# Kernel tuning notes

Measured on AMD Instinct MI355X. Metric: run time of the kernel, lower is better.

## Reference

```python
import jax, jax.numpy as jnp
import numpy as np

N, E, G = 131072, 2097152, 512
IN, H = 64, 2
C1, C2 = 32, 64
EDIM = 3
EPS = 1e-5


def setup_inputs() -> dict:
    key = jax.random.key(0)
    ks = jax.random.split(key, 32)
    p = lambda k, shp, s=0.1: (jax.random.normal(k, shp, dtype=jnp.float32) * s)
    inp = {
        'x': jax.random.normal(ks[0], (N, IN), dtype=jnp.float32),
        'edge_attr': jax.random.normal(ks[1], (E, EDIM), dtype=jnp.float32),
        # layer 1 (in=64 -> H*C1=64)
        'w1l': p(ks[2], (IN, H * C1)), 'b1l': p(ks[3], (H * C1,)),
        'w1r': p(ks[4], (IN, H * C1)), 'b1r': p(ks[5], (H * C1,)),
        'w1e': p(ks[6], (EDIM, H * C1)),
        'att1': p(ks[7], (H, C1)), 'bias1': p(ks[8], (C1,)),
        'g1': jnp.ones((C1,), jnp.float32), 'be1': jnp.zeros((C1,), jnp.float32),
        # layer 2 (in=32 -> H*C2=128)
        'w2l': p(ks[9], (C1, H * C2)), 'b2l': p(ks[10], (H * C2,)),
        'w2r': p(ks[11], (C1, H * C2)), 'b2r': p(ks[12], (H * C2,)),
        'w2e': p(ks[13], (EDIM, H * C2)),
        'att2': p(ks[14], (H, C2)), 'bias2': p(ks[15], (C2,)),
        'g2': jnp.ones((C2,), jnp.float32), 'be2': jnp.zeros((C2,), jnp.float32),
        # head
        'fc1w': p(ks[16], (C2, 32)), 'fc1b': p(ks[17], (32,)),
        'g3': jnp.ones((32,), jnp.float32), 'be3': jnp.zeros((32,), jnp.float32),
        'fc2w': p(ks[18], (32, 1)), 'fc2b': p(ks[19], (1,)),
        # graph structure (int)
        'edge_index': jax.random.randint(ks[20], (2, E), 0, N, dtype=jnp.int32),
        'batch': jnp.sort(jax.random.randint(ks[21], (N,), 0, G, dtype=jnp.int32)),
    }
    return inp


def _seg_softmax(logits, seg, n):
    # numerically stable segment softmax over edges grouped by dst node
    m = jax.ops.segment_max(logits, seg, num_segments=n)
    m = jnp.where(jnp.isfinite(m), m, 0.0)
    e = jnp.exp(logits - m[seg])
    s = jax.ops.segment_sum(e, seg, num_segments=n)
    return e / (s[seg] + 1e-16)


def _gatv2(x, src, dst, eattr, wl, bl, wr, br, we, att, bias, heads, ch):
    n = x.shape[0]
    xl = (x @ wl + bl).reshape(n, heads, ch)            # lin_l (source side)
    xr = (x @ wr + br).reshape(n, heads, ch)            # lin_r (target side)
    ee = (eattr @ we).reshape(-1, heads, ch)            # edge embedding
    m = jax.nn.leaky_relu(xl[src] + xr[dst] + ee, 0.2)  # [Etot,H,C]
    logits = jnp.einsum('ehc,hc->eh', m, att)           # [Etot,H]
    alpha = _seg_softmax(logits, dst, n)                # [Etot,H]
    out = jax.ops.segment_sum(alpha[:, :, None] * xl[src], dst, num_segments=n)
    return out.mean(axis=1) + bias                      # concat=False -> head mean


def _bn(x, g, b):
    mu = x.mean(0)
    v = x.var(0)
    return (x - mu) * jax.lax.rsqrt(v + EPS) * g + b


def reference(x, edge_attr, w1l, b1l, w1r, b1r, w1e, att1, bias1, g1, be1,
              w2l, b2l, w2r, b2r, w2e, att2, bias2, g2, be2,
              fc1w, fc1b, g3, be3, fc2w, fc2b, edge_index, batch):
    n = x.shape[0]
    src, dst = edge_index[0], edge_index[1]
    # add self loops with fill_value='mean' edge attrs (PyG default)
    cnt = jax.ops.segment_sum(jnp.ones_like(dst, jnp.float32), dst, num_segments=n)
    loop_attr = jax.ops.segment_sum(edge_attr, dst, num_segments=n) / jnp.maximum(cnt, 1.0)[:, None]
    ar = jnp.arange(n, dtype=src.dtype)
    src_f = jnp.concatenate([src, ar])
    dst_f = jnp.concatenate([dst, ar])
    ea_f = jnp.concatenate([edge_attr, loop_attr], axis=0)

    h = _gatv2(x, src_f, dst_f, ea_f, w1l, b1l, w1r, b1r, w1e, att1, bias1, H, C1)
    h = jax.nn.elu(_bn(h, g1, be1))
    h = _gatv2(h, src_f, dst_f, ea_f, w2l, b2l, w2r, b2r, w2e, att2, bias2, H, C2)
    h = jax.nn.elu(_bn(h, g2, be2))

    # global mean pool over graphs
    gs = jax.ops.segment_sum(h, batch, num_segments=G)
    gc = jax.ops.segment_sum(jnp.ones((n,), jnp.float32), batch, num_segments=G)
    pooled = gs / jnp.maximum(gc, 1.0)[:, None]

    z = jax.nn.elu(_bn(pooled @ fc1w + fc1b, g3, be3))
    return jax.nn.sigmoid(z @ fc2w + fc2b)
```

## Files before the change

### kernel.cpp

```cpp
#include <hip/hip_runtime.h>
#include <math.h>

#define NN 131072
#define EE 2097152
#define ET (EE + NN)
#define GG 512
#define BN_EPS 1e-5f

__device__ __forceinline__ unsigned short f2bf(float f) {
  unsigned u = __float_as_uint(f);
  u += 0x7fffu + ((u >> 16) & 1u);
  return (unsigned short)(u >> 16);
}
__device__ __forceinline__ float bf_lo(unsigned u) {
  return __uint_as_float(u << 16);
}
__device__ __forceinline__ float bf_hi(unsigned u) {
  return __uint_as_float(u & 0xffff0000u);
}

__global__ void k_hist(const int* __restrict__ ei, int* __restrict__ cnt,
                       int* __restrict__ rank) {
  int e = blockIdx.x * blockDim.x + threadIdx.x;
  if (e >= EE) return;
  rank[e] = atomicAdd(&cnt[ei[EE + e]], 1);
}

__global__ void k_scan_a(const int* __restrict__ cnt, int* __restrict__ off_out,
                         int* __restrict__ bsum) {
  __shared__ int s[256];
  int i = blockIdx.x * 256 + threadIdx.x;
  int x = cnt[i] + 1;
  s[threadIdx.x] = x;
  __syncthreads();
#pragma unroll
  for (int o = 1; o < 256; o <<= 1) {
    int t = (threadIdx.x >= o) ? s[threadIdx.x - o] : 0;
    __syncthreads();
    s[threadIdx.x] += t;
    __syncthreads();
  }
  off_out[i] = s[threadIdx.x] - x;
  if (threadIdx.x == 255) bsum[blockIdx.x] = s[255];
}

__global__ void k_scan_b(int* __restrict__ bsum) {
  __shared__ int s[512];
  int t = threadIdx.x;
  int x = bsum[t];
  s[t] = x;
  __syncthreads();
#pragma unroll
  for (int o = 1; o < 512; o <<= 1) {
    int v = (t >= o) ? s[t - o] : 0;
    __syncthreads();
    s[t] += v;
    __syncthreads();
  }
  bsum[t] = s[t] - x;
}

__global__ void k_scan_c(int* __restrict__ off_out, const int* __restrict__ bsum) {
  int i = blockIdx.x * 256 + threadIdx.x;
  off_out[i] += bsum[blockIdx.x];
  if (i == 0) off_out[NN] = ET;
}

__global__ void k_scatter(const int* __restrict__ ei, const float* __restrict__ ea,
                          const int* __restrict__ off, const int* __restrict__ rank,
                          float4* __restrict__ ces) {
  int e = blockIdx.x * blockDim.x + threadIdx.x;
  if (e >= EE) return;
  int s = ei[e], d = ei[EE + e];
  int p = off[d] + rank[e];
  float4 t = {ea[3 * e], ea[3 * e + 1], ea[3 * e + 2], __int_as_float(s)};
  ces[p] = t;
}

__global__ void k_selfslot(const int* __restrict__ off, float4* __restrict__ ces) {
  int tid = blockIdx.x * blockDim.x + threadIdx.x;
  int wave = tid >> 6;
  int lane = threadIdx.x & 63;
  int grp = lane >> 4;
  int gl = lane & 15;
  int v = wave * 4 + grp;
  if (v >= NN) return;
  int b = off[v];
  int d = off[v + 1] - b - 1;
  float s0 = 0.f, s1 = 0.f, s2 = 0.f;
  for (int j = gl; j < d; j += 16) {
    float4 t = ces[b + j];
    s0 += t.x;
    s1 += t.y;
    s2 += t.z;
  }
#pragma unroll
  for (int m = 1; m <= 8; m <<= 1) {
    s0 += __shfl_xor(s0, m, 64);
    s1 += __shfl_xor(s1, m, 64);
    s2 += __shfl_xor(s2, m, 64);
  }
  if (gl == 0) {
    float inv = 1.0f / (float)(d > 0 ? d : 1);
    float4 t = {s0 * inv, s1 * inv, s2 * inv, __int_as_float(v)};
    ces[b + d] = t;
  }
}

template <int K, int O, bool DO_BN>
__global__ void k_lin(const float* __restrict__ x, const float* __restrict__ wl,
                      const float* __restrict__ bl, const float* __restrict__ wr,
                      const float* __restrict__ br, unsigned short* __restrict__ xlb,
                      float* __restrict__ xr, const float* __restrict__ bnsum,
                      const float* __restrict__ bnss, const float* __restrict__ g,
                      const float* __restrict__ be) {
  constexpr int NPB = 256 / O;
  __shared__ float swl[K * O], swr[K * O], sx[NPB * K];
  __shared__ float sscale[K], sshift[K];
  for (int i = threadIdx.x; i < K * O; i += 256) {
    swl[i] = wl[i];
    swr[i] = wr[i];
  }
  if (DO_BN && threadIdx.x < K) {
    int c = threadIdx.x;
    float mu = bnsum[c] * (1.0f / NN);
    float var = bnss[c] * (1.0f / NN) - mu * mu;
    float is = rsqrtf(var + BN_EPS) * g[c];
    sscale[c] = is;
    sshift[c] = be[c] - mu * is;
  }
  int o = threadIdx.x % O;
  int ln = threadIdx.x / O;
  float blv = bl[o], brv = br[o];
  __syncthreads();
  for (int v0 = blockIdx.x * NPB; v0 < NN; v0 += gridDim.x * NPB) {
    __syncthreads();
    for (int i = threadIdx.x; i < NPB * K; i += 256) {
      float xv = x[(size_t)v0 * K + i];
      if (DO_BN) {
        int c = i & (K - 1);
        xv = xv * sscale[c] + sshift[c];
        xv = (xv > 0.0f) ? xv : (__expf(xv) - 1.0f);
      }
      sx[i] = xv;
    }
    __syncthreads();
    float al = blv, ar = brv;
#pragma unroll 8
    for (int k = 0; k < K; k++) {
      float xv = sx[ln * K + k];
      al += xv * swl[k * O + o];
      ar += xv * swr[k * O + o];
    }
    int v = v0 + ln;
    xlb[(size_t)v * O + o] = f2bf(al);
    xr[(size_t)v * O + o] = ar;
  }
}


__global__ void k_gat128(const int* __restrict__ off, const float4* __restrict__ ces,
                         const uint2* __restrict__ xlb, const float4* __restrict__ xr,
                         const float4* __restrict__ we, const float4* __restrict__ att,
                         const float4* __restrict__ bias, float4* __restrict__ hout,
                         float* __restrict__ bnsum, float* __restrict__ bnss) {
  __shared__ float lsum[4][64], lsq[4][64];
  int lane = threadIdx.x & 63;
  int wid = threadIdx.x >> 6;
  int cl = lane & 31;
  int half = lane >> 5;
  const float4 w0 = we[cl], w1 = we[32 + cl], w2 = we[64 + cl];
  const float4 av = att[cl];
  float4 rs = {0, 0, 0, 0}, rq = {0, 0, 0, 0};
  for (int v = blockIdx.x * 4 + wid; v < NN; v += gridDim.x * 4) {
    int b = off[v], e = off[v + 1];
    int last = e - 1;
    float4 xrv = xr[(size_t)v * 32 + cl];
    float ssum = 0.0f;
    float4 acc = {0, 0, 0, 0};
    int ng = (e - b + 3) >> 2;
    int j = b;
    float4 pa = ces[min(j + half, last)];
    float4 pb = ces[min(j + 2 + half, last)];
    uint2 ua = xlb[(size_t)__float_as_int(pa.w) * 32 + cl];
    uint2 ub = xlb[(size_t)__float_as_int(pb.w) * 32 + cl];
    float4 qa = ces[min(j + 4 + half, last)];
    float4 qb = ces[min(j + 6 + half, last)];
    for (int g = 0; g < ng; g++, j += 4) {
      uint2 nua = xlb[(size_t)__float_as_int(qa.w) * 32 + cl];
      uint2 nub = xlb[(size_t)__float_as_int(qb.w) * 32 + cl];
      float4 ta = ces[min(j + 8 + half, last)];
      float4 tb = ces[min(j + 10 + half, last)];
      float4 ra, rb;
      ra.x = bf_lo(ua.x); ra.y = bf_hi(ua.x); ra.z = bf_lo(ua.y); ra.w = bf_hi(ua.y);
      rb.x = bf_lo(ub.x); rb.y = bf_hi(ub.x); rb.z = bf_lo(ub.y); rb.w = bf_hi(ub.y);
      float4 ma, mb;
      ma.x = ra.x + xrv.x + pa.x * w0.x + pa.y * w1.x + pa.z * w2.x;
      ma.y = ra.y + xrv.y + pa.x * w0.y + pa.y * w1.y + pa.z * w2.y;
      ma.z = ra.z + xrv.z + pa.x * w0.z + pa.y * w1.z + pa.z * w2.z;
      ma.w = ra.w + xrv.w + pa.x * w0.w + pa.y * w1.w + pa.z * w2.w;
      mb.x = rb.x + xrv.x + pb.x * w0.x + pb.y * w1.x + pb.z * w2.x;
      mb.y = rb.y + xrv.y + pb.x * w0.y + pb.y * w1.y + pb.z * w2.y;
      mb.z = rb.z + xrv.z + pb.x * w0.z + pb.y * w1.z + pb.z * w2.z;
      mb.w = rb.w + xrv.w + pb.x * w0.w + pb.y * w1.w + pb.z * w2.w;
      ma.x = fmaxf(ma.x, 0.2f * ma.x); ma.y = fmaxf(ma.y, 0.2f * ma.y);
      ma.z = fmaxf(ma.z, 0.2f * ma.z); ma.w = fmaxf(ma.w, 0.2f * ma.w);
      mb.x = fmaxf(mb.x, 0.2f * mb.x); mb.y = fmaxf(mb.y, 0.2f * mb.y);
      mb.z = fmaxf(mb.z, 0.2f * mb.z); mb.w = fmaxf(mb.w, 0.2f * mb.w);
      float la = ma.x * av.x + ma.y * av.y + ma.z * av.z + ma.w * av.w;
      float lb = mb.x * av.x + mb.y * av.y + mb.z * av.z + mb.w * av.w;
#pragma unroll
      for (int m = 1; m <= 8; m <<= 1) {
        la += __shfl_xor(la, m, 64);
        lb += __shfl_xor(lb, m, 64);
      }
      float pA = ((j + half) < e) ? __expf(la) : 0.0f;
      float pB = ((j + 2 + half) < e) ? __expf(lb) : 0.0f;
      ssum += pA + pB;
      acc.x += pA * ra.x + pB * rb.x;
      acc.y += pA * ra.y + pB * rb.y;
      acc.z += pA * ra.z + pB * rb.z;
      acc.w += pA * ra.w + pB * rb.w;
      pa = qa; pb = qb; ua = nua; ub = nub; qa = ta; qb = tb;
    }
    ssum += __shfl_xor(ssum, 32, 64);
    acc.x += __shfl_xor(acc.x, 32, 64);
    acc.y += __shfl_xor(acc.y, 32, 64);
    acc.z += __shfl_xor(acc.z, 32, 64);
    acc.w += __shfl_xor(acc.w, 32, 64);
    float inv = 1.0f / (ssum + 1e-16f);
    float4 o = {acc.x * inv, acc.y * inv, acc.z * inv, acc.w * inv};
    float px = __shfl_xor(o.x, 16, 64);
    float py = __shfl_xor(o.y, 16, 64);
    float pz = __shfl_xor(o.z, 16, 64);
    float pw = __shfl_xor(o.w, 16, 64);
    if (lane < 16) {
      float4 bv = bias[lane];
      float4 val = {0.5f * (o.x + px) + bv.x, 0.5f * (o.y + py) + bv.y,
                    0.5f * (o.z + pz) + bv.z, 0.5f * (o.w + pw) + bv.w};
      hout[(size_t)v * 16 + lane] = val;
      rs.x += val.x; rs.y += val.y; rs.z += val.z; rs.w += val.w;
      rq.x += val.x * val.x; rq.y += val.y * val.y;
      rq.z += val.z * val.z; rq.w += val.w * val.w;
    }
  }
  if (lane < 16) {
    lsum[wid][4 * lane] = rs.x; lsum[wid][4 * lane + 1] = rs.y;
    lsum[wid][4 * lane + 2] = rs.z; lsum[wid][4 * lane + 3] = rs.w;
    lsq[wid][4 * lane] = rq.x; lsq[wid][4 * lane + 1] = rq.y;
    lsq[wid][4 * lane + 2] = rq.z; lsq[wid][4 * lane + 3] = rq.w;
  }
  __syncthreads();
  if (threadIdx.x < 64) {
    float a = lsum[0][threadIdx.x] + lsum[1][threadIdx.x] + lsum[2][threadIdx.x] +
              lsum[3][threadIdx.x];
    float q = lsq[0][threadIdx.x] + lsq[1][threadIdx.x] + lsq[2][threadIdx.x] +
              lsq[3][threadIdx.x];
    atomicAdd(&bnsum[threadIdx.x], a);
    atomicAdd(&bnss[threadIdx.x], q);
  }
}

__global__ void k_gat64(const int* __restrict__ off, const float4* __restrict__ ces,
                        const unsigned* __restrict__ xlb, const float2* __restrict__ xr,
                        const float2* __restrict__ we, const float2* __restrict__ att,
                        const float2* __restrict__ bias, float2* __restrict__ hout,
                        float* __restrict__ bnsum, float* __restrict__ bnss) {
  __shared__ float lsum[4][32], lsq[4][32];
  int lane = threadIdx.x & 63;
  int wid = threadIdx.x >> 6;
  int cl = lane & 31;
  int half = lane >> 5;
  const float2 w0 = we[cl], w1 = we[32 + cl], w2 = we[64 + cl];
  const float2 av = att[cl];
  float2 rs = {0, 0}, rq = {0, 0};
  for (int v = blockIdx.x * 4 + wid; v < NN; v += gridDim.x * 4) {
    int b = off[v], e = off[v + 1];
    int last = e - 1;
    float2 xrv = xr[(size_t)v * 32 + cl];
    float ssum = 0.0f;
    float2 acc = {0, 0};
    int ng = (e - b + 3) >> 2;
    int j = b;
    float4 pa = ces[min(j + half, last)];
    float4 pb = ces[min(j + 2 + half, last)];
    unsigned ua = xlb[(size_t)__float_as_int(pa.w) * 32 + cl];
    unsigned ub = xlb[(size_t)__float_as_int(pb.w) * 32 + cl];
    float4 qa = ces[min(j + 4 + half, last)];
    float4 qb = ces[min(j + 6 + half, last)];
    for (int g = 0; g < ng; g++, j += 4) {
      unsigned nua = xlb[(size_t)__float_as_int(qa.w) * 32 + cl];
      unsigned nub = xlb[(size_t)__float_as_int(qb.w) * 32 + cl];
      float4 ta = ces[min(j + 8 + half, last)];
      float4 tb = ces[min(j + 10 + half, last)];
      float2 ra = {bf_lo(ua), bf_hi(ua)};
      float2 rb = {bf_lo(ub), bf_hi(ub)};
      float2 ma, mb;
      ma.x = ra.x + xrv.x + pa.x * w0.x + pa.y * w1.x + pa.z * w2.x;
      ma.y = ra.y + xrv.y + pa.x * w0.y + pa.y * w1.y + pa.z * w2.y;
      mb.x = rb.x + xrv.x + pb.x * w0.x + pb.y * w1.x + pb.z * w2.x;
      mb.y = rb.y + xrv.y + pb.x * w0.y + pb.y * w1.y + pb.z * w2.y;
      ma.x = fmaxf(ma.x, 0.2f * ma.x); ma.y = fmaxf(ma.y, 0.2f * ma.y);
      mb.x = fmaxf(mb.x, 0.2f * mb.x); mb.y = fmaxf(mb.y, 0.2f * mb.y);
      float la = ma.x * av.x + ma.y * av.y;
      float lb = mb.x * av.x + mb.y * av.y;
#pragma unroll
      for (int m = 1; m <= 8; m <<= 1) {
        la += __shfl_xor(la, m, 64);
        lb += __shfl_xor(lb, m, 64);
      }
      float pA = ((j + half) < e) ? __expf(la) : 0.0f;
      float pB = ((j + 2 + half) < e) ? __expf(lb) : 0.0f;
      ssum += pA + pB;
      acc.x += pA * ra.x + pB * rb.x;
      acc.y += pA * ra.y + pB * rb.y;
      pa = qa; pb = qb; ua = nua; ub = nub; qa = ta; qb = tb;
    }
    ssum += __shfl_xor(ssum, 32, 64);
    acc.x += __shfl_xor(acc.x, 32, 64);
    acc.y += __shfl_xor(acc.y, 32, 64);
    float inv = 1.0f / (ssum + 1e-16f);
    float2 o = {acc.x * inv, acc.y * inv};
    float px = __shfl_xor(o.x, 16, 64);
    float py = __shfl_xor(o.y, 16, 64);
    if (lane < 16) {
      float2 bv = bias[lane];
      float2 val = {0.5f * (o.x + px) + bv.x, 0.5f * (o.y + py) + bv.y};
      hout[(size_t)v * 16 + lane] = val;
      rs.x += val.x; rs.y += val.y;
      rq.x += val.x * val.x; rq.y += val.y * val.y;
    }
  }
  if (lane < 16) {
    lsum[wid][2 * lane] = rs.x; lsum[wid][2 * lane + 1] = rs.y;
    lsq[wid][2 * lane] = rq.x; lsq[wid][2 * lane + 1] = rq.y;
  }
  __syncthreads();
  if (threadIdx.x < 32) {
    float a = lsum[0][threadIdx.x] + lsum[1][threadIdx.x] + lsum[2][threadIdx.x] +
              lsum[3][threadIdx.x];
    float q = lsq[0][threadIdx.x] + lsq[1][threadIdx.x] + lsq[2][threadIdx.x] +
              lsq[3][threadIdx.x];
    atomicAdd(&bnsum[threadIdx.x], a);
    atomicAdd(&bnss[threadIdx.x], q);
  }
}

__global__ void k_goffbs(const int* __restrict__ batch, int* __restrict__ goff) {
  int g = threadIdx.x;
  int lo = 0, hi = NN;
  while (lo < hi) {
    int mid = (lo + hi) >> 1;
    if (batch[mid] < g) lo = mid + 1; else hi = mid;
  }
  goff[g] = lo;
  if (g == 0) goff[GG] = NN;
}

__global__ void k_pool(const float* __restrict__ h2, const int* __restrict__ goff,
                       const float* __restrict__ bnsum, const float* __restrict__ bnss,
                       const float* __restrict__ g, const float* __restrict__ be,
                       float* __restrict__ pooled) {
  int gi = blockIdx.x, c = threadIdx.x;
  float mu = bnsum[c] * (1.0f / NN);
  float var = bnss[c] * (1.0f / NN) - mu * mu;
  float is = rsqrtf(var + BN_EPS) * g[c];
  float sh = be[c] - mu * is;
  int s = goff[gi], n = goff[gi + 1] - s;
  float acc = 0.0f;
  int i = 0;
  for (; i + 4 <= n; i += 4) {
    float y0 = h2[(size_t)(s + i) * 64 + c];
    float y1 = h2[(size_t)(s + i + 1) * 64 + c];
    float y2 = h2[(size_t)(s + i + 2) * 64 + c];
    float y3 = h2[(size_t)(s + i + 3) * 64 + c];
    y0 = y0 * is + sh; y1 = y1 * is + sh; y2 = y2 * is + sh; y3 = y3 * is + sh;
    y0 = (y0 > 0.0f) ? y0 : (__expf(y0) - 1.0f);
    y1 = (y1 > 0.0f) ? y1 : (__expf(y1) - 1.0f);
    y2 = (y2 > 0.0f) ? y2 : (__expf(y2) - 1.0f);
    y3 = (y3 > 0.0f) ? y3 : (__expf(y3) - 1.0f);
    acc += (y0 + y1) + (y2 + y3);
  }
  for (; i < n; i++) {
    float y = h2[(size_t)(s + i) * 64 + c] * is + sh;
    y = (y > 0.0f) ? y : (__expf(y) - 1.0f);
    acc += y;
  }
  pooled[gi * 64 + c] = acc / fmaxf((float)n, 1.0f);
}

__global__ void k_fc1(const float* __restrict__ pooled, const float* __restrict__ w,
                      const float* __restrict__ b, float* __restrict__ t1) {
  int i = blockIdx.x * blockDim.x + threadIdx.x;
  int g = i >> 5, o = i & 31;
  float acc = b[o];
#pragma unroll 8
  for (int k = 0; k < 64; k++) acc += pooled[g * 64 + k] * w[k * 32 + o];
  t1[i] = acc;
}

__global__ void k_head(const float* __restrict__ t1, const float* __restrict__ g3,
                       const float* __restrict__ be3, const float* __restrict__ fc2w,
                       const float* __restrict__ fc2b, float* __restrict__ out) {
  __shared__ float ssum[32], ssq[32], smu[32], sinv[32];
  int t = threadIdx.x;
  if (t < 32) {
    ssum[t] = 0.0f;
    ssq[t] = 0.0f;
  }
  __syncthreads();
  float y[32];
#pragma unroll
  for (int o = 0; o < 32; o++) y[o] = t1[t * 32 + o];
#pragma unroll
  for (int o = 0; o < 32; o++) {
    atomicAdd(&ssum[o], y[o]);
    atomicAdd(&ssq[o], y[o] * y[o]);
  }
  __syncthreads();
  if (t < 32) {
    float mu = ssum[t] * (1.0f / GG);
    float var = ssq[t] * (1.0f / GG) - mu * mu;
    smu[t] = mu;
    sinv[t] = rsqrtf(var + BN_EPS);
  }
  __syncthreads();
  float acc = fc2b[0];
#pragma unroll
  for (int o = 0; o < 32; o++) {
    float yy = (y[o] - smu[o]) * sinv[o] * g3[o] + be3[o];
    yy = (yy > 0.0f) ? yy : (__expf(yy) - 1.0f);
    acc += yy * fc2w[o];
  }
  out[t] = 1.0f / (1.0f + __expf(-acc));
}

extern "C" void kernel_launch(void* const* d_in, const int* in_sizes, int n_in,
                              void* d_out, int out_size, void* d_ws, size_t ws_size,
                              hipStream_t stream) {
  const float* x = (const float*)d_in[0];
  const float* ea = (const float*)d_in[1];
  const float* w1l = (const float*)d_in[2];
  const float* b1l = (const float*)d_in[3];
  const float* w1r = (const float*)d_in[4];
  const float* b1r = (const float*)d_in[5];
  const float* w1e = (const float*)d_in[6];
  const float* att1 = (const float*)d_in[7];
  const float* bias1 = (const float*)d_in[8];
  const float* g1 = (const float*)d_in[9];
  const float* be1 = (const float*)d_in[10];
  const float* w2l = (const float*)d_in[11];
  const float* b2l = (const float*)d_in[12];
  const float* w2r = (const float*)d_in[13];
  const float* b2r = (const float*)d_in[14];
  const float* w2e = (const float*)d_in[15];
  const float* att2 = (const float*)d_in[16];
  const float* bias2 = (const float*)d_in[17];
  const float* g2 = (const float*)d_in[18];
  const float* be2 = (const float*)d_in[19];
  const float* fc1w = (const float*)d_in[20];
  const float* fc1b = (const float*)d_in[21];
  const float* g3 = (const float*)d_in[22];
  const float* be3 = (const float*)d_in[23];
  const float* fc2w = (const float*)d_in[24];
  const float* fc2b = (const float*)d_in[25];
  const int* ei = (const int*)d_in[26];
  const int* batch = (const int*)d_in[27];
  float* out = (float*)d_out;

  char* w = (char*)d_ws;
  size_t off = 0;
  auto alloc = [&](size_t bytes) {
    size_t r = off;
    off += (bytes + 255) & ~(size_t)255;
    return r;
  };
  int* cnt = (int*)(w + alloc(NN * 4));
  float* bn1sum = (float*)(w + alloc(32 * 4));
  float* bn1ss = (float*)(w + alloc(32 * 4));
  float* bn2sum = (float*)(w + alloc(64 * 4));
  float* bn2ss = (float*)(w + alloc(64 * 4));
  size_t zero_bytes = off;
  int* rank = (int*)(w + alloc((size_t)EE * 4));
  int* csr_off = (int*)(w + alloc((size_t)(NN + 1) * 4));
  int* bsum = (int*)(w + alloc(512 * 4));
  int* goff = (int*)(w + alloc((size_t)(GG + 1) * 4));
  float4* ces = (float4*)(w + alloc((size_t)ET * 16));
  unsigned short* xlb = (unsigned short*)(w + alloc((size_t)NN * 128 * 2));
  float* xr = (float*)(w + alloc((size_t)NN * 128 * 4));
  float* h1 = (float*)(w + alloc((size_t)NN * 32 * 4));
  float* h2 = (float*)(w + alloc((size_t)NN * 64 * 4));
  float* pooled = (float*)(w + alloc((size_t)GG * 64 * 4));
  float* t1 = (float*)(w + alloc((size_t)GG * 32 * 4));
  (void)ws_size;
  (void)in_sizes;
  (void)n_in;
  (void)out_size;

  hipMemsetAsync(d_ws, 0, zero_bytes, stream);

  k_hist<<<EE / 256, 256, 0, stream>>>(ei, cnt, rank);
  k_scan_a<<<512, 256, 0, stream>>>(cnt, csr_off, bsum);
  k_scan_b<<<1, 512, 0, stream>>>(bsum);
  k_scan_c<<<512, 256, 0, stream>>>(csr_off, bsum);
  k_scatter<<<EE / 256, 256, 0, stream>>>(ei, ea, csr_off, rank, ces);
  k_selfslot<<<NN / 16, 256, 0, stream>>>(csr_off, ces);

  k_lin<64, 64, false><<<2048, 256, 0, stream>>>(x, w1l, b1l, w1r, b1r, xlb, xr,
                                                 nullptr, nullptr, nullptr, nullptr);
  k_gat64<<<2048, 256, 0, stream>>>(csr_off, ces, (const unsigned*)xlb,
                                    (const float2*)xr, (const float2*)w1e,
                                    (const float2*)att1, (const float2*)bias1,
                                    (float2*)h1, bn1sum, bn1ss);

  k_lin<32, 128, true><<<2048, 256, 0, stream>>>(h1, w2l, b2l, w2r, b2r, xlb, xr,
                                                 bn1sum, bn1ss, g1, be1);
  k_gat128<<<2048, 256, 0, stream>>>(csr_off, ces, (const uint2*)xlb,
                                     (const float4*)xr, (const float4*)w2e,
                                     (const float4*)att2, (const float4*)bias2,
                                     (float4*)h2, bn2sum, bn2ss);

  k_goffbs<<<1, GG, 0, stream>>>(batch, goff);
  k_pool<<<GG, 64, 0, stream>>>(h2, goff, bn2sum, bn2ss, g2, be2, pooled);
  k_fc1<<<64, 256, 0, stream>>>(pooled, fc1w, fc1b, t1);
  k_head<<<1, GG, 0, stream>>>(t1, g3, be3, fc2w, fc2b, out);
}
```

Measured before the change: 990.2 us.

## Remap GAT aggregation lanes to 16 per edge with wider vector gathers

Both GAT aggregation kernels now give 16 lanes to each edge and process four edges per wave at once, instead of 32 lanes per edge with two edges per half-wave. Each lane loads wider bf16 and fp32 vectors, which cuts the per-edge attention-logit reduction to three shuffles. The min() clamping on prefetch indices is removed; instead the CSR edge array gets 16 zeroed padding slots, so prefetches past the end stay in bounds and stray edges are masked by the jj<e check. This trades more registers per lane (two float4 accumulators in the 128-wide kernel) for fewer shuffle and index instructions and better-coalesced gathers.

```diff
diff --git a/kernel.cpp b/kernel.cpp
--- a/kernel.cpp
+++ b/kernel.cpp
@@ -12,12 +12,8 @@
   u += 0x7fffu + ((u >> 16) & 1u);
   return (unsigned short)(u >> 16);
 }
-__device__ __forceinline__ float bf_lo(unsigned u) {
-  return __uint_as_float(u << 16);
-}
-__device__ __forceinline__ float bf_hi(unsigned u) {
-  return __uint_as_float(u & 0xffff0000u);
-}
+__device__ __forceinline__ float bf_lo(unsigned u) { return __uint_as_float(u << 16); }
+__device__ __forceinline__ float bf_hi(unsigned u) { return __uint_as_float(u & 0xffff0000u); }
 
 __global__ void k_hist(const int* __restrict__ ei, int* __restrict__ cnt,
                        int* __restrict__ rank) {
@@ -79,6 +75,10 @@
 
 __global__ void k_selfslot(const int* __restrict__ off, float4* __restrict__ ces) {
   int tid = blockIdx.x * blockDim.x + threadIdx.x;
+  if (tid < 16) {
+    float4 z = {0.0f, 0.0f, 0.0f, __int_as_float(0)};
+    ces[ET + tid] = z;
+  }
   int wave = tid >> 6;
   int lane = threadIdx.x & 63;
   int grp = lane >> 4;
@@ -160,95 +160,101 @@
 
 
 __global__ void k_gat128(const int* __restrict__ off, const float4* __restrict__ ces,
-                         const uint2* __restrict__ xlb, const float4* __restrict__ xr,
+                         const uint4* __restrict__ xlb, const float4* __restrict__ xr,
                          const float4* __restrict__ we, const float4* __restrict__ att,
                          const float4* __restrict__ bias, float4* __restrict__ hout,
                          float* __restrict__ bnsum, float* __restrict__ bnss) {
   __shared__ float lsum[4][64], lsq[4][64];
   int lane = threadIdx.x & 63;
   int wid = threadIdx.x >> 6;
-  int cl = lane & 31;
-  int half = lane >> 5;
-  const float4 w0 = we[cl], w1 = we[32 + cl], w2 = we[64 + cl];
-  const float4 av = att[cl];
-  float4 rs = {0, 0, 0, 0}, rq = {0, 0, 0, 0};
+  int el = lane & 15;
+  int st = lane >> 4;
+  const float4 w0a = we[el * 2], w0b = we[el * 2 + 1];
+  const float4 w1a = we[32 + el * 2], w1b = we[32 + el * 2 + 1];
+  const float4 w2a = we[64 + el * 2], w2b = we[64 + el * 2 + 1];
+  const float4 ava = att[el * 2], avb = att[el * 2 + 1];
+  float4 rsa = {0, 0, 0, 0}, rsb = {0, 0, 0, 0};
+  float4 rqa = {0, 0, 0, 0}, rqb = {0, 0, 0, 0};
   for (int v = blockIdx.x * 4 + wid; v < NN; v += gridDim.x * 4) {
     int b = off[v], e = off[v + 1];
-    int last = e - 1;
-    float4 xrv = xr[(size_t)v * 32 + cl];
+    float4 xra = xr[(size_t)v * 32 + el * 2];
+    float4 xrb = xr[(size_t)v * 32 + el * 2 + 1];
     float ssum = 0.0f;
-    float4 acc = {0, 0, 0, 0};
+    float4 acca = {0, 0, 0, 0}, accb = {0, 0, 0, 0};
     int ng = (e - b + 3) >> 2;
-    int j = b;
-    float4 pa = ces[min(j + half, last)];
-    float4 pb = ces[min(j + 2 + half, last)];
-    uint2 ua = xlb[(size_t)__float_as_int(pa.w) * 32 + cl];
-    uint2 ub = xlb[(size_t)__float_as_int(pb.w) * 32 + cl];
-    float4 qa = ces[min(j + 4 + half, last)];
-    float4 qb = ces[min(j + 6 + half, last)];
-    for (int g = 0; g < ng; g++, j += 4) {
-      uint2 nua = xlb[(size_t)__float_as_int(qa.w) * 32 + cl];
-      uint2 nub = xlb[(size_t)__float_as_int(qb.w) * 32 + cl];
-      float4 ta = ces[min(j + 8 + half, last)];
-      float4 tb = ces[min(j + 10 + half, last)];
+    int jj = b + st;
+    float4 pa = ces[jj];
+    uint4 ua = xlb[(size_t)__float_as_int(pa.w) * 16 + el];
+    float4 qa = ces[jj + 4];
+    for (int g = 0; g < ng; g++) {
+      uint4 nua = xlb[(size_t)__float_as_int(qa.w) * 16 + el];
+      float4 ta = ces[jj + 8];
       float4 ra, rb;
       ra.x = bf_lo(ua.x); ra.y = bf_hi(ua.x); ra.z = bf_lo(ua.y); ra.w = bf_hi(ua.y);
-      rb.x = bf_lo(ub.x); rb.y = bf_hi(ub.x); rb.z = bf_lo(ub.y); rb.w = bf_hi(ub.y);
+      rb.x = bf_lo(ua.z); rb.y = bf_hi(ua.z); rb.z = bf_lo(ua.w); rb.w = bf_hi(ua.w);
       float4 ma, mb;
-      ma.x = ra.x + xrv.x + pa.x * w0.x + pa.y * w1.x + pa.z * w2.x;
-      ma.y = ra.y + xrv.y + pa.x * w0.y + pa.y * w1.y + pa.z * w2.y;
-      ma.z = ra.z + xrv.z + pa.x * w0.z + pa.y * w1.z + pa.z * w2.z;
-      ma.w = ra.w + xrv.w + pa.x * w0.w + pa.y * w1.w + pa.z * w2.w;
-      mb.x = rb.x + xrv.x + pb.x * w0.x + pb.y * w1.x + pb.z * w2.x;
-      mb.y = rb.y + xrv.y + pb.x * w0.y + pb.y * w1.y + pb.z * w2.y;
-      mb.z = rb.z + xrv.z + pb.x * w0.z + pb.y * w1.z + pb.z * w2.z;
-      mb.w = rb.w + xrv.w + pb.x * w0.w + pb.y * w1.w + pb.z * w2.w;
+      ma.x = ra.x + xra.x + pa.x * w0a.x + pa.y * w1a.x + pa.z * w2a.x;
+      ma.y = ra.y + xra.y + pa.x * w0a.y + pa.y * w1a.y + pa.z * w2a.y;
+      ma.z = ra.z + xra.z + pa.x * w0a.z + pa.y * w1a.z + pa.z * w2a.z;
+      ma.w = ra.w + xra.w + pa.x * w0a.w + pa.y * w1a.w + pa.z * w2a.w;
+      mb.x = rb.x + xrb.x + pa.x * w0b.x + pa.y * w1b.x + pa.z * w2b.x;
+      mb.y = rb.y + xrb.y + pa.x * w0b.y + pa.y * w1b.y + pa.z * w2b.y;
+      mb.z = rb.z + xrb.z + pa.x * w0b.z + pa.y * w1b.z + pa.z * w2b.z;
+      mb.w = rb.w + xrb.w + pa.x * w0b.w + pa.y * w1b.w + pa.z * w2b.w;
       ma.x = fmaxf(ma.x, 0.2f * ma.x); ma.y = fmaxf(ma.y, 0.2f * ma.y);
       ma.z = fmaxf(ma.z, 0.2f * ma.z); ma.w = fmaxf(ma.w, 0.2f * ma.w);
       mb.x = fmaxf(mb.x, 0.2f * mb.x); mb.y = fmaxf(mb.y, 0.2f * mb.y);
       mb.z = fmaxf(mb.z, 0.2f * mb.z); mb.w = fmaxf(mb.w, 0.2f * mb.w);
-      float la = ma.x * av.x + ma.y * av.y + ma.z * av.z + ma.w * av.w;
-      float lb = mb.x * av.x + mb.y * av.y + mb.z * av.z + mb.w * av.w;
-#pragma unroll
-      for (int m = 1; m <= 8; m <<= 1) {
-        la += __shfl_xor(la, m, 64);
-        lb += __shfl_xor(lb, m, 64);
-      }
-      float pA = ((j + half) < e) ? __expf(la) : 0.0f;
-      float pB = ((j + 2 + half) < e) ? __expf(lb) : 0.0f;
-      ssum += pA + pB;
-      acc.x += pA * ra.x + pB * rb.x;
-      acc.y += pA * ra.y + pB * rb.y;
-      acc.z += pA * ra.z + pB * rb.z;
-      acc.w += pA * ra.w + pB * rb.w;
-      pa = qa; pb = qb; ua = nua; ub = nub; qa = ta; qb = tb;
-    }
-    ssum += __shfl_xor(ssum, 32, 64);
-    acc.x += __shfl_xor(acc.x, 32, 64);
-    acc.y += __shfl_xor(acc.y, 32, 64);
-    acc.z += __shfl_xor(acc.z, 32, 64);
-    acc.w += __shfl_xor(acc.w, 32, 64);
+      float l = ma.x * ava.x + ma.y * ava.y + ma.z * ava.z + ma.w * ava.w +
+                mb.x * avb.x + mb.y * avb.y + mb.z * avb.z + mb.w * avb.w;
+      l += __shfl_xor(l, 1, 64);
+      l += __shfl_xor(l, 2, 64);
+      l += __shfl_xor(l, 4, 64);
+      float p = (jj < e) ? __expf(l) : 0.0f;
+      ssum += p;
+      acca.x += p * ra.x; acca.y += p * ra.y; acca.z += p * ra.z; acca.w += p * ra.w;
+      accb.x += p * rb.x; accb.y += p * rb.y; accb.z += p * rb.z; accb.w += p * rb.w;
+      jj += 4;
+      pa = qa; ua = nua; qa = ta;
+    }
+#pragma unroll
+    for (int m = 16; m <= 32; m <<= 1) {
+      ssum += __shfl_xor(ssum, m, 64);
+      acca.x += __shfl_xor(acca.x, m, 64); acca.y += __shfl_xor(acca.y, m, 64);
+      acca.z += __shfl_xor(acca.z, m, 64); acca.w += __shfl_xor(acca.w, m, 64);
+      accb.x += __shfl_xor(accb.x, m, 64); accb.y += __shfl_xor(accb.y, m, 64);
+      accb.z += __shfl_xor(accb.z, m, 64); accb.w += __shfl_xor(accb.w, m, 64);
+    }
     float inv = 1.0f / (ssum + 1e-16f);
-    float4 o = {acc.x * inv, acc.y * inv, acc.z * inv, acc.w * inv};
-    float px = __shfl_xor(o.x, 16, 64);
-    float py = __shfl_xor(o.y, 16, 64);
-    float pz = __shfl_xor(o.z, 16, 64);
-    float pw = __shfl_xor(o.w, 16, 64);
-    if (lane < 16) {
-      float4 bv = bias[lane];
-      float4 val = {0.5f * (o.x + px) + bv.x, 0.5f * (o.y + py) + bv.y,
-                    0.5f * (o.z + pz) + bv.z, 0.5f * (o.w + pw) + bv.w};
-      hout[(size_t)v * 16 + lane] = val;
-      rs.x += val.x; rs.y += val.y; rs.z += val.z; rs.w += val.w;
-      rq.x += val.x * val.x; rq.y += val.y * val.y;
-      rq.z += val.z * val.z; rq.w += val.w * val.w;
-    }
-  }
-  if (lane < 16) {
-    lsum[wid][4 * lane] = rs.x; lsum[wid][4 * lane + 1] = rs.y;
-    lsum[wid][4 * lane + 2] = rs.z; lsum[wid][4 * lane + 3] = rs.w;
-    lsq[wid][4 * lane] = rq.x; lsq[wid][4 * lane + 1] = rq.y;
-    lsq[wid][4 * lane + 2] = rq.z; lsq[wid][4 * lane + 3] = rq.w;
+    float4 oa = {acca.x * inv, acca.y * inv, acca.z * inv, acca.w * inv};
+    float4 ob = {accb.x * inv, accb.y * inv, accb.z * inv, accb.w * inv};
+    float pax = __shfl_xor(oa.x, 8, 64), pay = __shfl_xor(oa.y, 8, 64);
+    float paz = __shfl_xor(oa.z, 8, 64), paw = __shfl_xor(oa.w, 8, 64);
+    float pbx = __shfl_xor(ob.x, 8, 64), pby = __shfl_xor(ob.y, 8, 64);
+    float pbz = __shfl_xor(ob.z, 8, 64), pbw = __shfl_xor(ob.w, 8, 64);
+    if (lane < 8) {
+      float4 bva = bias[el * 2], bvb = bias[el * 2 + 1];
+      float4 va = {0.5f * (oa.x + pax) + bva.x, 0.5f * (oa.y + pay) + bva.y,
+                   0.5f * (oa.z + paz) + bva.z, 0.5f * (oa.w + paw) + bva.w};
+      float4 vb = {0.5f * (ob.x + pbx) + bvb.x, 0.5f * (ob.y + pby) + bvb.y,
+                   0.5f * (ob.z + pbz) + bvb.z, 0.5f * (ob.w + pbw) + bvb.w};
+      hout[(size_t)v * 16 + el * 2] = va;
+      hout[(size_t)v * 16 + el * 2 + 1] = vb;
+      rsa.x += va.x; rsa.y += va.y; rsa.z += va.z; rsa.w += va.w;
+      rsb.x += vb.x; rsb.y += vb.y; rsb.z += vb.z; rsb.w += vb.w;
+      rqa.x += va.x * va.x; rqa.y += va.y * va.y; rqa.z += va.z * va.z; rqa.w += va.w * va.w;
+      rqb.x += vb.x * vb.x; rqb.y += vb.y * vb.y; rqb.z += vb.z * vb.z; rqb.w += vb.w * vb.w;
+    }
+  }
+  if (lane < 8) {
+    lsum[wid][el * 8 + 0] = rsa.x; lsum[wid][el * 8 + 1] = rsa.y;
+    lsum[wid][el * 8 + 2] = rsa.z; lsum[wid][el * 8 + 3] = rsa.w;
+    lsum[wid][el * 8 + 4] = rsb.x; lsum[wid][el * 8 + 5] = rsb.y;
+    lsum[wid][el * 8 + 6] = rsb.z; lsum[wid][el * 8 + 7] = rsb.w;
+    lsq[wid][el * 8 + 0] = rqa.x; lsq[wid][el * 8 + 1] = rqa.y;
+    lsq[wid][el * 8 + 2] = rqa.z; lsq[wid][el * 8 + 3] = rqa.w;
+    lsq[wid][el * 8 + 4] = rqb.x; lsq[wid][el * 8 + 5] = rqb.y;
+    lsq[wid][el * 8 + 6] = rqb.z; lsq[wid][el * 8 + 7] = rqb.w;
   }
   __syncthreads();
   if (threadIdx.x < 64) {
@@ -262,78 +268,75 @@
 }
 
 __global__ void k_gat64(const int* __restrict__ off, const float4* __restrict__ ces,
-                        const unsigned* __restrict__ xlb, const float2* __restrict__ xr,
-                        const float2* __restrict__ we, const float2* __restrict__ att,
-                        const float2* __restrict__ bias, float2* __restrict__ hout,
+                        const uint2* __restrict__ xlb, const float4* __restrict__ xr,
+                        const float4* __restrict__ we, const float4* __restrict__ att,
+                        const float4* __restrict__ bias, float4* __restrict__ hout,
                         float* __restrict__ bnsum, float* __restrict__ bnss) {
   __shared__ float lsum[4][32], lsq[4][32];
   int lane = threadIdx.x & 63;
   int wid = threadIdx.x >> 6;
-  int cl = lane & 31;
-  int half = lane >> 5;
-  const float2 w0 = we[cl], w1 = we[32 + cl], w2 = we[64 + cl];
-  const float2 av = att[cl];
-  float2 rs = {0, 0}, rq = {0, 0};
+  int el = lane & 15;
+  int st = lane >> 4;
+  const float4 w0 = we[el], w1 = we[16 + el], w2 = we[32 + el];
+  const float4 av = att[el];
+  float4 rs = {0, 0, 0, 0}, rq = {0, 0, 0, 0};
   for (int v = blockIdx.x * 4 + wid; v < NN; v += gridDim.x * 4) {
     int b = off[v], e = off[v + 1];
-    int last = e - 1;
-    float2 xrv = xr[(size_t)v * 32 + cl];
+    float4 xrv = xr[(size_t)v * 16 + el];
     float ssum = 0.0f;
-    float2 acc = {0, 0};
+    float4 acc = {0, 0, 0, 0};
     int ng = (e - b + 3) >> 2;
-    int j = b;
-    float4 pa = ces[min(j + half, last)];
-    float4 pb = ces[min(j + 2 + half, last)];
-    unsigned ua = xlb[(size_t)__float_as_int(pa.w) * 32 + cl];
-    unsigned ub = xlb[(size_t)__float_as_int(pb.w) * 32 + cl];
-    float4 qa = ces[min(j + 4 + half, last)];
-    float4 qb = ces[min(j + 6 + half, last)];
-    for (int g = 0; g < ng; g++, j += 4) {
-      unsigned nua = xlb[(size_t)__float_as_int(qa.w) * 32 + cl];
-      unsigned nub = xlb[(size_t)__float_as_int(qb.w) * 32 + cl];
-      float4 ta = ces[min(j + 8 + half, last)];
-      float4 tb = ces[min(j + 10 + half, last)];
-      float2 ra = {bf_lo(ua), bf_hi(ua)};
-      float2 rb = {bf_lo(ub), bf_hi(ub)};
-      float2 ma, mb;
+    int jj = b + st;
+    float4 pa = ces[jj];
+    uint2 ua = xlb[(size_t)__float_as_int(pa.w) * 16 + el];
+    float4 qa = ces[jj + 4];
+    for (int g = 0; g < ng; g++) {
+      uint2 nua = xlb[(size_t)__float_as_int(qa.w) * 16 + el];
+      float4 ta = ces[jj + 8];
+      float4 ra;
+      ra.x = bf_lo(ua.x); ra.y = bf_hi(ua.x); ra.z = bf_lo(ua.y); ra.w = bf_hi(ua.y);
+      float4 ma;
       ma.x = ra.x + xrv.x + pa.x * w0.x + pa.y * w1.x + pa.z * w2.x;
       ma.y = ra.y + xrv.y + pa.x * w0.y + pa.y * w1.y + pa.z * w2.y;
-      mb.x = rb.x + xrv.x + pb.x * w0.x + pb.y * w1.x + pb.z * w2.x;
-      mb.y = rb.y + xrv.y + pb.x * w0.y + pb.y * w1.y + pb.z * w2.y;
+      ma.z = ra.z + xrv.z + pa.x * w0.z + pa.y * w1.z + pa.z * w2.z;
+      ma.w = ra.w + xrv.w + pa.x * w0.w + pa.y * w1.w + pa.z * w2.w;
       ma.x = fmaxf(ma.x, 0.2f * ma.x); ma.y = fmaxf(ma.y, 0.2f * ma.y);
-      mb.x = fmaxf(mb.x, 0.2f * mb.x); mb.y = fmaxf(mb.y, 0.2f * mb.y);
-      float la = ma.x * av.x + ma.y * av.y;
-      float lb = mb.x * av.x + mb.y * av.y;
-#pragma unroll
-      for (int m = 1; m <= 8; m <<= 1) {
-        la += __shfl_xor(la, m, 64);
-        lb += __shfl_xor(lb, m, 64);
-      }
-      float pA = ((j + half) < e) ? __expf(la) : 0.0f;
-      float pB = ((j + 2 + half) < e) ? __expf(lb) : 0.0f;
-      ssum += pA + pB;
-      acc.x += pA * ra.x + pB * rb.x;
-      acc.y += pA * ra.y + pB * rb.y;
-      pa = qa; pb = qb; ua = nua; ub = nub; qa = ta; qb = tb;
-    }
-    ssum += __shfl_xor(ssum, 32, 64);
-    acc.x += __shfl_xor(acc.x, 32, 64);
-    acc.y += __shfl_xor(acc.y, 32, 64);
+      ma.z = fmaxf(ma.z, 0.2f * ma.z); ma.w = fmaxf(ma.w, 0.2f * ma.w);
+      float l = ma.x * av.x + ma.y * av.y + ma.z * av.z + ma.w * av.w;
+      l += __shfl_xor(l, 1, 64);
+      l += __shfl_xor(l, 2, 64);
+      l += __shfl_xor(l, 4, 64);
+      float p = (jj < e) ? __expf(l) : 0.0f;
+      ssum += p;
+      acc.x += p * ra.x; acc.y += p * ra.y; acc.z += p * ra.z; acc.w += p * ra.w;
+      jj += 4;
+      pa = qa; ua = nua; qa = ta;
+    }
+#pragma unroll
+    for (int m = 16; m <= 32; m <<= 1) {
+      ssum += __shfl_xor(ssum, m, 64);
+      acc.x += __shfl_xor(acc.x, m, 64); acc.y += __shfl_xor(acc.y, m, 64);
+      acc.z += __shfl_xor(acc.z, m, 64); acc.w += __shfl_xor(acc.w, m, 64);
+    }
     float inv = 1.0f / (ssum + 1e-16f);
-    float2 o = {acc.x * inv, acc.y * inv};
-    float px = __shfl_xor(o.x, 16, 64);
-    float py = __shfl_xor(o.y, 16, 64);
-    if (lane < 16) {
-      float2 bv = bias[lane];
-      float2 val = {0.5f * (o.x + px) + bv.x, 0.5f * (o.y + py) + bv.y};
-      hout[(size_t)v * 16 + lane] = val;
-      rs.x += val.x; rs.y += val.y;
+    float4 o = {acc.x * inv, acc.y * inv, acc.z * inv, acc.w * inv};
+    float px = __shfl_xor(o.x, 8, 64), py = __shfl_xor(o.y, 8, 64);
+    float pz = __shfl_xor(o.z, 8, 64), pw = __shfl_xor(o.w, 8, 64);
+    if (lane < 8) {
+      float4 bv = bias[el];
+      float4 val = {0.5f * (o.x + px) + bv.x, 0.5f * (o.y + py) + bv.y,
+                    0.5f * (o.z + pz) + bv.z, 0.5f * (o.w + pw) + bv.w};
+      hout[(size_t)v * 8 + el] = val;
+      rs.x += val.x; rs.y += val.y; rs.z += val.z; rs.w += val.w;
       rq.x += val.x * val.x; rq.y += val.y * val.y;
-    }
-  }
-  if (lane < 16) {
-    lsum[wid][2 * lane] = rs.x; lsum[wid][2 * lane + 1] = rs.y;
-    lsq[wid][2 * lane] = rq.x; lsq[wid][2 * lane + 1] = rq.y;
+      rq.z += val.z * val.z; rq.w += val.w * val.w;
+    }
+  }
+  if (lane < 8) {
+    lsum[wid][el * 4 + 0] = rs.x; lsum[wid][el * 4 + 1] = rs.y;
+    lsum[wid][el * 4 + 2] = rs.z; lsum[wid][el * 4 + 3] = rs.w;
+    lsq[wid][el * 4 + 0] = rq.x; lsq[wid][el * 4 + 1] = rq.y;
+    lsq[wid][el * 4 + 2] = rq.z; lsq[wid][el * 4 + 3] = rq.w;
   }
   __syncthreads();
   if (threadIdx.x < 32) {
@@ -485,7 +488,7 @@
   int* csr_off = (int*)(w + alloc((size_t)(NN + 1) * 4));
   int* bsum = (int*)(w + alloc(512 * 4));
   int* goff = (int*)(w + alloc((size_t)(GG + 1) * 4));
-  float4* ces = (float4*)(w + alloc((size_t)ET * 16));
+  float4* ces = (float4*)(w + alloc((size_t)(ET + 16) * 16));
   unsigned short* xlb = (unsigned short*)(w + alloc((size_t)NN * 128 * 2));
   float* xr = (float*)(w + alloc((size_t)NN * 128 * 4));
   float* h1 = (float*)(w + alloc((size_t)NN * 32 * 4));
@@ -508,14 +511,14 @@
 
   k_lin<64, 64, false><<<2048, 256, 0, stream>>>(x, w1l, b1l, w1r, b1r, xlb, xr,
                                                  nullptr, nullptr, nullptr, nullptr);
-  k_gat64<<<2048, 256, 0, stream>>>(csr_off, ces, (const unsigned*)xlb,
-                                    (const float2*)xr, (const float2*)w1e,
-                                    (const float2*)att1, (const float2*)bias1,
-                                    (float2*)h1, bn1sum, bn1ss);
+  k_gat64<<<2048, 256, 0, stream>>>(csr_off, ces, (const uint2*)xlb,
+                                    (const float4*)xr, (const float4*)w1e,
+                                    (const float4*)att1, (const float4*)bias1,
+                                    (float4*)h1, bn1sum, bn1ss);
 
   k_lin<32, 128, true><<<2048, 256, 0, stream>>>(h1, w2l, b2l, w2r, b2r, xlb, xr,
                                                  bn1sum, bn1ss, g1, be1);
-  k_gat128<<<2048, 256, 0, stream>>>(csr_off, ces, (const uint2*)xlb,
+  k_gat128<<<2048, 256, 0, stream>>>(csr_off, ces, (const uint4*)xlb,
                                      (const float4*)xr, (const float4*)w2e,
                                      (const float4*)att2, (const float4*)bias2,
                                      (float4*)h2, bn2sum, bn2ss);
```

New measurement: 952.4 us. 3.8% less time.
